# Kernel tuning notes

Hardware: AMD Instinct MI355X
Metric: run time of the kernel (lower is better)

Reference implementation:

```python
import jax, jax.numpy as jnp
import numpy as np

H = 8            # num_heads
HID = 128        # hidden_channels
D = HID // H     # per-head dim
L = 2            # num_layers
NCLS = 4         # out_channels (number of 1-class heads)


def _forward(x_a, x_b, lin_W_a, lin_b_a, lin_W_b, lin_b_b,
             Wk, bk, Wq, bq, Wv, bv, arel, mrel, prel,
             Wa, ba_out, skip, Wcls, bcls, edges):
    """HGT forward. edges: list of (src_type, dst_type, [2,E] int array); list
    position is the relation index into arel/mrel/prel."""
    # per-type input projection + ReLU
    x = [jax.nn.relu(x_a @ lin_W_a + lin_b_a),
         jax.nn.relu(x_b @ lin_W_b + lin_b_b)]
    N = [x[0].shape[0], x[1].shape[0]]
    scale = 1.0 / np.sqrt(D)
    for l in range(L):
        # per-type K/Q/V projections -> [N, H, D]
        k = [(x[t] @ Wk[l, t] + bk[l, t]).reshape(N[t], H, D) for t in range(2)]
        q = [(x[t] @ Wq[l, t] + bq[l, t]).reshape(N[t], H, D) for t in range(2)]
        v = [(x[t] @ Wv[l, t] + bv[l, t]).reshape(N[t], H, D) for t in range(2)]
        new_x = []
        for dt in range(2):
            logits, vals, dsts = [], [], []
            for r, (s_t, d_t, ei) in enumerate(edges):
                if d_t != dt:
                    continue
                src, dst = ei[0], ei[1]
                # relation-specific per-head transforms of gathered src K/V
                ke = jnp.einsum('ehd,hdf->ehf', k[s_t][src], arel[l, r])  # [E,H,D]
                ve = jnp.einsum('ehd,hdf->ehf', v[s_t][src], mrel[l, r])  # [E,H,D]
                a = jnp.sum(q[dt][dst] * ke, axis=-1) * prel[l, r] * scale  # [E,H]
                logits.append(a); vals.append(ve); dsts.append(dst)
            a = jnp.concatenate(logits, axis=0)
            ve = jnp.concatenate(vals, axis=0)
            dst = jnp.concatenate(dsts, axis=0)
            # segment softmax over all incoming edges per destination node
            amax = jax.ops.segment_max(a, dst, num_segments=N[dt])           # [N,H]
            ae = jnp.exp(a - amax[dst])                                       # [E,H]
            den = jax.ops.segment_sum(ae, dst, num_segments=N[dt])           # [N,H]
            msg = jax.ops.segment_sum(ae[:, :, None] * ve, dst,
                                      num_segments=N[dt])                    # [N,H,D]
            out = (msg / jnp.maximum(den, 1e-16)[:, :, None]).reshape(N[dt], HID)
            # output projection with GELU + learned skip gate
            out = jax.nn.gelu(out) @ Wa[l, dt] + ba_out[l, dt]
            beta = jax.nn.sigmoid(skip[l, dt])
            new_x.append(beta * out + (1.0 - beta) * x[dt])
        x = new_x
    # node_to_predict == 'a'; concatenated 1-class heads -> [Na, NCLS]
    return x[0] @ Wcls.T + bcls


def setup_inputs() -> dict:
    key = jax.random.key(0)
    ks = iter(jax.random.split(key, 40))
    Na, Nb, E = 50000, 50000, 150000
    def rn(shape, fan_in):
        return jax.random.normal(next(ks), shape, dtype=jnp.float32) / np.sqrt(fan_in)
    inp = {
        'x_a': jax.random.normal(next(ks), (Na, 64), dtype=jnp.float32),
        'x_b': jax.random.normal(next(ks), (Nb, 32), dtype=jnp.float32),
        'lin_W_a': rn((64, HID), 64), 'lin_b_a': jnp.zeros((HID,), jnp.float32),
        'lin_W_b': rn((32, HID), 32), 'lin_b_b': jnp.zeros((HID,), jnp.float32),
        'Wk': rn((L, 2, HID, HID), HID), 'bk': jnp.zeros((L, 2, HID), jnp.float32),
        'Wq': rn((L, 2, HID, HID), HID), 'bq': jnp.zeros((L, 2, HID), jnp.float32),
        'Wv': rn((L, 2, HID, HID), HID), 'bv': jnp.zeros((L, 2, HID), jnp.float32),
        'arel': rn((L, 4, H, D, D), D), 'mrel': rn((L, 4, H, D, D), D),
        'prel': jnp.ones((L, 4, H), jnp.float32),
        'Wa': rn((L, 2, HID, HID), HID), 'ba_out': jnp.zeros((L, 2, HID), jnp.float32),
        'skip': jnp.ones((L, 2), jnp.float32),
        'Wcls': rn((NCLS, HID), HID), 'bcls': jnp.zeros((NCLS,), jnp.float32),
        'edge_aa': jax.random.randint(next(ks), (2, E), 0, Na, dtype=jnp.int32),
        'edge_ab': jax.random.randint(next(ks), (2, E), 0, Na, dtype=jnp.int32),
        'edge_ba': jax.random.randint(next(ks), (2, E), 0, Na, dtype=jnp.int32),
        'edge_bb': jax.random.randint(next(ks), (2, E), 0, Nb, dtype=jnp.int32),
    }
    return inp


def reference(x_a, x_b, lin_W_a, lin_b_a, lin_W_b, lin_b_b,
              Wk, bk, Wq, bq, Wv, bv, arel, mrel, prel,
              Wa, ba_out, skip, Wcls, bcls,
              edge_aa, edge_ab, edge_ba, edge_bb):
    edges = [(0, 0, edge_aa), (0, 1, edge_ab), (1, 0, edge_ba), (1, 1, edge_bb)]
    return _forward(x_a, x_b, lin_W_a, lin_b_a, lin_W_b, lin_b_b,
                    Wk, bk, Wq, bq, Wv, bv, arel, mrel, prel,
                    Wa, ba_out, skip, Wcls, bcls, edges)
```

## Files before the change

### kernel.cpp

```cpp
#include <hip/hip_runtime.h>
#include <math.h>

#define HIDC 128
#define NH 8
#define HD 16
#define NCLS 4

typedef __attribute__((ext_vector_type(8))) short s8v;
typedef __attribute__((ext_vector_type(4))) float f4v;

#define ST_STRIDE 264
#define ST_BYTES  (64 * ST_STRIDE * 2)

__device__ __forceinline__ float gelu_f(float h) {
    float z = 0.7978845608028654f * (h + 0.044715f * h * h * h);
    float t = 1.f - 2.f / (1.f + __expf(2.f * z));
    return 0.5f * h * (1.f + t);
}
__device__ __forceinline__ unsigned short f2bf(float x) {
    unsigned b = __float_as_uint(x);
    unsigned r = (b + 0x7FFFu + ((b >> 16) & 1u)) >> 16;
    return (unsigned short)r;
}
__device__ __forceinline__ float bf2f(unsigned short u) {
    return __uint_as_float(((unsigned)u) << 16);
}
__device__ __forceinline__ void gload_lds16(const void* g, void* l) {
    __builtin_amdgcn_global_load_lds(
        (const __attribute__((address_space(1))) unsigned int*)g,
        (__attribute__((address_space(3))) unsigned int*)l, 16, 0, 0);
}

__global__ void zero_u32(unsigned* __restrict__ p, long n)
{
    long i = (long)blockIdx.x * blockDim.x + threadIdx.x;
    long stride = (long)gridDim.x * blockDim.x;
    for (; i < n; i += stride) p[i] = 0u;
}

__global__ void fold_all(const float* __restrict__ Wk, const float* __restrict__ bk,
                         const float* __restrict__ Wv, const float* __restrict__ bv,
                         const float* __restrict__ arel, const float* __restrict__ mrel,
                         float* __restrict__ Wt, float* __restrict__ bt)
{
    __shared__ float rsh[NH * HD * HD];
    int bid = blockIdx.x;
    int w = bid & 1, r = (bid >> 1) & 3, l = bid >> 3;
    int st = r >> 1;
    const float* W   = (w ? Wv : Wk) + (size_t)(l * 2 + st) * HIDC * HIDC;
    const float* bb  = (w ? bv : bk) + (size_t)(l * 2 + st) * HIDC;
    const float* rel = (w ? mrel : arel) + (size_t)(l * 4 + r) * NH * HD * HD;
    float* wt  = Wt + (size_t)bid * HIDC * HIDC;
    float* btp = bt + (size_t)bid * HIDC;

    int t = threadIdx.x;
    for (int i = t; i < NH * HD * HD; i += 128) rsh[i] = rel[i];
    __syncthreads();
    int h = t >> 4, f = t & 15;
    const float* rh = rsh + h * HD * HD + f;
    for (int k = 0; k < HIDC; ++k) {
        float acc = 0.f;
        const float* wr = W + (size_t)k * HIDC + h * HD;
        #pragma unroll
        for (int d = 0; d < HD; ++d) acc = fmaf(wr[d], rh[d * HD], acc);
        wt[(size_t)k * HIDC + t] = acc;
    }
    float accb = 0.f;
    const float* br = bb + h * HD;
    #pragma unroll
    for (int d = 0; d < HD; ++d) accb = fmaf(br[d], rh[d * HD], accb);
    btp[t] = accb;
}

__global__ __launch_bounds__(128)
void wsplit(const float* __restrict__ linWa, const float* __restrict__ linWb,
            const float* __restrict__ Wq, const float* __restrict__ Wa,
            const float* __restrict__ Wt, unsigned short* __restrict__ W2,
            int Ka, int Kb)
{
    int bid = blockIdx.x;
    int nka = Ka >> 5, nkb = Kb >> 5;
    const float* src; size_t moff; int ks, Km;
    if (bid < nka) { src = linWa; moff = 0; ks = bid; Km = Ka; }
    else if (bid < nka + nkb) { src = linWb; moff = (size_t)2 * Ka * 128; ks = bid - nka; Km = Kb; }
    else {
        int cc = bid - nka - nkb;
        int mm = cc >> 2; ks = cc & 3; Km = 128;
        moff = (size_t)2 * (Ka + Kb) * 128 + (size_t)mm * 32768;
        if (mm < 16)      src = Wt + (size_t)mm * 16384;
        else if (mm < 20) src = Wq + (size_t)(mm - 16) * 16384;
        else              src = Wa + (size_t)(mm - 20) * 16384;
    }
    int t = threadIdx.x;
    int fn = t >> 4, lr = t & 15;
    for (int g = 0; g < 4; ++g)
        for (int j = 0; j < 8; ++j) {
            int k = ks * 32 + g * 8 + j;
            float x = src[(size_t)k * 128 + fn * 16 + lr];
            unsigned short h = f2bf(x);
            size_t co = moff + (size_t)ks * 4096 + fn * 512 + g * 128 + lr * 8 + j;
            W2[co] = h;
            W2[co + (size_t)Km * 128] = f2bf(x - bf2f(h));
        }
}

__global__ void hist4(const int* __restrict__ d0, int E0, const int* __restrict__ d1, int E1,
                      const int* __restrict__ d2, int E2, const int* __restrict__ d3, int E3,
                      unsigned* __restrict__ cnt, int Nmax)
{
    int i = blockIdx.x * blockDim.x + threadIdx.x;
    int tot = E0 + E1 + E2 + E3;
    int stride = gridDim.x * blockDim.x;
    for (; i < tot; i += stride) {
        int j = i; const int* p; int dt;
        if (j < E0) { p = d0; dt = 0; }
        else { j -= E0;
            if (j < E1) { p = d1; dt = 1; }
            else { j -= E1;
                if (j < E2) { p = d2; dt = 0; }
                else { j -= E2; p = d3; dt = 1; }
            }
        }
        atomicAdd(&cnt[(size_t)dt * Nmax + p[j]], 1u);
    }
}

__global__ __launch_bounds__(256)
void scan_p1(const unsigned* __restrict__ cnt, unsigned* __restrict__ bsum,
             int Nmax, int nblk, int n0, int n1)
{
    int ty = blockIdx.x / nblk, b = blockIdx.x % nblk;
    int n = ty ? n1 : n0;
    const unsigned* c = cnt + (size_t)ty * Nmax;
    int i0 = b * 1024 + threadIdx.x * 4;
    unsigned s = 0;
    #pragma unroll
    for (int j = 0; j < 4; ++j) { int i = i0 + j; if (i < n) s += c[i]; }
    __shared__ unsigned sh[256];
    sh[threadIdx.x] = s; __syncthreads();
    for (int off = 128; off; off >>= 1) {
        if (threadIdx.x < (unsigned)off) sh[threadIdx.x] += sh[threadIdx.x + off];
        __syncthreads();
    }
    if (threadIdx.x == 0) bsum[blockIdx.x] = sh[0];
}

__global__ __launch_bounds__(256)
void scan_p2(unsigned* __restrict__ bsum, int nblk, int* __restrict__ rowptr,
             int Nmax, int n0, int n1)
{
    __shared__ unsigned sh[256];
    int tot = 2 * nblk;
    int t = threadIdx.x;
    unsigned v = (t < tot) ? bsum[t] : 0u;
    sh[t] = v; __syncthreads();
    for (int off = 1; off < 256; off <<= 1) {
        unsigned add = (t >= off) ? sh[t - off] : 0u;
        __syncthreads(); sh[t] += add; __syncthreads();
    }
    unsigned t0 = sh[nblk - 1];
    unsigned tall = sh[255];
    unsigned excl = sh[t] - v;
    if (t < tot) bsum[t] = (t < nblk) ? excl : excl - t0;
    if (t == 0) {
        rowptr[n0] = (int)t0;
        rowptr[(Nmax + 1) + n1] = (int)(tall - t0);
    }
}

__global__ __launch_bounds__(256)
void scan_p3(const unsigned* __restrict__ cnt, const unsigned* __restrict__ bsum,
             int* __restrict__ rowptr, unsigned* __restrict__ cursor,
             int Nmax, int nblk, int n0, int n1)
{
    int ty = blockIdx.x / nblk, b = blockIdx.x % nblk;
    int n = ty ? n1 : n0;
    const unsigned* c = cnt + (size_t)ty * Nmax;
    int* rp = rowptr + (size_t)ty * (Nmax + 1);
    unsigned* cur = cursor + (size_t)ty * Nmax;
    int t = threadIdx.x;
    int i0 = b * 1024 + t * 4;
    unsigned v[4]; unsigned s = 0;
    #pragma unroll
    for (int j = 0; j < 4; ++j) { int i = i0 + j; v[j] = (i < n) ? c[i] : 0u; s += v[j]; }
    __shared__ unsigned sh[256];
    sh[t] = s; __syncthreads();
    for (int off = 1; off < 256; off <<= 1) {
        unsigned add = (t >= off) ? sh[t - off] : 0u;
        __syncthreads(); sh[t] += add; __syncthreads();
    }
    unsigned run = bsum[blockIdx.x] + sh[t] - s;
    #pragma unroll
    for (int j = 0; j < 4; ++j) {
        int i = i0 + j;
        if (i < n) { rp[i] = (int)run; cur[i] = run; }
        run += v[j];
    }
}

__global__ void scatter4(const int* __restrict__ e0, int E0, const int* __restrict__ e1, int E1,
                         const int* __restrict__ e2, int E2, const int* __restrict__ e3, int E3,
                         unsigned* __restrict__ cursor, int Nmax,
                         unsigned* __restrict__ adj0, unsigned* __restrict__ adj1)
{
    int i = blockIdx.x * blockDim.x + threadIdx.x;
    int tot = E0 + E1 + E2 + E3;
    int stride = gridDim.x * blockDim.x;
    for (; i < tot; i += stride) {
        int j = i; const int* e; int E; int dt; unsigned rb;
        if (j < E0) { e = e0; E = E0; dt = 0; rb = 0u; }
        else { j -= E0;
            if (j < E1) { e = e1; E = E1; dt = 1; rb = 0u; }
            else { j -= E1;
                if (j < E2) { e = e2; E = E2; dt = 0; rb = 1u << 24; }
                else { j -= E2; e = e3; E = E3; dt = 1; rb = 1u << 24; }
            }
        }
        int s = e[j], d = e[E + j];
        unsigned pos = atomicAdd(&cursor[(size_t)dt * Nmax + d], 1u);
        (dt ? adj1 : adj0)[pos] = (unsigned)s | rb;
    }
}

template <int ASPLIT, int EPI, int OUT, int NK>
__global__ __launch_bounds__(256)
void mg2p(const void* __restrict__ Ain, const unsigned short* __restrict__ Whi,
          const float* __restrict__ bias,
          const unsigned short* __restrict__ xold, const float* __restrict__ skipp,
          void* __restrict__ Cout, int N)
{
    constexpr int K = NK * 32;
    constexpr int PB = NK * 8192;
    constexpr size_t LSZ = (OUT == 2 && ST_BYTES > PB) ? ST_BYTES : PB;
    __shared__ char ldsraw[LSZ];
    unsigned short* lds = (unsigned short*)ldsraw;
    int t = threadIdx.x;
    constexpr int NCP = PB / (16 * 256);
    #pragma unroll
    for (int i = 0; i < NCP; ++i)
        gload_lds16((const char*)Whi + ((size_t)t + i * 256) * 16,
                    ldsraw + ((size_t)t + i * 256) * 16);
    __syncthreads();

    int w = t >> 6, lane = t & 63;
    int lr = lane & 15, g = lane >> 4;
    int row0 = blockIdx.x * 64;
    int fnb = w * 2;

    f4v acc[4][2];
    #pragma unroll
    for (int i = 0; i < 4; ++i) { acc[i][0] = (f4v)0.f; acc[i][1] = (f4v)0.f; }

    #pragma unroll
    for (int ks = 0; ks < NK; ++ks) {
        s8v ah[4], al[4];
        #pragma unroll
        for (int fm = 0; fm < 4; ++fm) {
            int row = row0 + fm * 16 + lr;
            if (row < N) {
                if (ASPLIT) {
                    const unsigned short* ap = (const unsigned short*)Ain + (size_t)row * 256 + ks * 32 + g * 8;
                    ah[fm] = *(const s8v*)ap;
                    al[fm] = *(const s8v*)(ap + 128);
                } else {
                    const float* ap = (const float*)Ain + (size_t)row * K + ks * 32 + g * 8;
                    float4 p = *(const float4*)ap;
                    float4 q = *(const float4*)(ap + 4);
                    float xv[8] = {p.x, p.y, p.z, p.w, q.x, q.y, q.z, q.w};
                    #pragma unroll
                    for (int j = 0; j < 8; ++j) {
                        unsigned short h = f2bf(xv[j]);
                        ah[fm][j] = (short)h;
                        al[fm][j] = (short)f2bf(xv[j] - bf2f(h));
                    }
                }
            } else { ah[fm] = (s8v)0; al[fm] = (s8v)0; }
        }
        #pragma unroll
        for (int f = 0; f < 2; ++f) {
            size_t co = (size_t)ks * 8192 + (fnb + f) * 1024 + g * 256 + lr * 16;
            s8v b = *(const s8v*)(ldsraw + co);
            #pragma unroll
            for (int fm = 0; fm < 4; ++fm) {
                acc[fm][f] = __builtin_amdgcn_mfma_f32_16x16x32_bf16(ah[fm], b, acc[fm][f], 0, 0, 0);
                acc[fm][f] = __builtin_amdgcn_mfma_f32_16x16x32_bf16(al[fm], b, acc[fm][f], 0, 0, 0);
            }
        }
    }

    float beta = 0.f;
    if (EPI == 2) beta = 1.f / (1.f + __expf(-skipp[0]));
    int rb = g * 4;

    if (OUT == 2) {
        __syncthreads();
        #pragma unroll
        for (int f = 0; f < 2; ++f) {
            int col = (fnb + f) * 16 + lr;
            float bv = bias[col];
            #pragma unroll
            for (int fm = 0; fm < 4; ++fm) {
                #pragma unroll
                for (int j = 0; j < 4; ++j) {
                    int lrow = fm * 16 + rb + j;
                    int row = row0 + lrow;
                    float o = acc[fm][f][j] + bv;
                    if (EPI == 1) o = fmaxf(o, 0.f);
                    if (EPI == 2) {
                        float xo = (row < N) ? (bf2f(xold[(size_t)row * 256 + col]) +
                                                bf2f(xold[(size_t)row * 256 + 128 + col])) : 0.f;
                        o = beta * o + (1.f - beta) * xo;
                    }
                    unsigned short h = f2bf(o);
                    lds[(size_t)lrow * ST_STRIDE + col] = h;
                    lds[(size_t)lrow * ST_STRIDE + 128 + col] = f2bf(o - bf2f(h));
                }
            }
        }
        __syncthreads();
        unsigned short* C = (unsigned short*)Cout;
        #pragma unroll
        for (int it = 0; it < 8; ++it) {
            int d4 = (it * 256 + t) * 4;
            int row = d4 >> 7, c2 = d4 & 127;
            int grow = row0 + row;
            if (grow < N) {
                uint4 v = *(const uint4*)(lds + (size_t)row * ST_STRIDE + c2 * 2);
                *(uint4*)(C + (size_t)grow * 256 + c2 * 2) = v;
            }
        }
    } else {
        float* C = (float*)Cout;
        #pragma unroll
        for (int f = 0; f < 2; ++f) {
            int col = (fnb + f) * 16 + lr;
            float bv = bias[col];
            #pragma unroll
            for (int fm = 0; fm < 4; ++fm) {
                #pragma unroll
                for (int j = 0; j < 4; ++j) {
                    int row = row0 + fm * 16 + rb + j;
                    if (row < N) C[(size_t)row * HIDC + col] = acc[fm][f][j] + bv;
                }
            }
        }
    }
}

struct KvArgs {
    const unsigned short* A[4];
    const unsigned short* Wm[4];
    const float* bias[4];
    unsigned short* out[4];
    int N[4];
    int cum[5];
};

__global__ __launch_bounds__(256)
void mgemm_kv4(KvArgs args)
{
    int bid = blockIdx.x;
    int jb = 0;
    while (jb < 3 && bid >= args.cum[jb + 1]) ++jb;
    int lb = bid - args.cum[jb];
    const unsigned short* Ain = args.A[jb];
    const unsigned short* Wkt = args.Wm[jb];
    const unsigned short* Wvt = args.Wm[jb] + 32768;
    const float* bias2 = args.bias[jb];
    unsigned short* kv = args.out[jb];
    int N = args.N[jb];

    __shared__ char ldsraw[65536];
    unsigned short* lds = (unsigned short*)ldsraw;
    int t = threadIdx.x;
    #pragma unroll
    for (int i = 0; i < 8; ++i)
        gload_lds16((const char*)Wkt + ((size_t)t + i * 256) * 16,
                    ldsraw + ((size_t)t + i * 256) * 16);
    #pragma unroll
    for (int i = 0; i < 8; ++i)
        gload_lds16((const char*)Wvt + ((size_t)t + i * 256) * 16,
                    ldsraw + 32768 + ((size_t)t + i * 256) * 16);

    int w = t >> 6, lane = t & 63;
    int lr = lane & 15, g = lane >> 4;
    int row0 = lb * 64;
    int fnb = w * 2;

    s8v ah[4][4], al[4][4];
    #pragma unroll
    for (int fm = 0; fm < 4; ++fm) {
        int row = row0 + fm * 16 + lr;
        #pragma unroll
        for (int ks = 0; ks < 4; ++ks) {
            if (row < N) {
                const unsigned short* ap = Ain + (size_t)row * 256 + ks * 32 + g * 8;
                ah[fm][ks] = *(const s8v*)ap;
                al[fm][ks] = *(const s8v*)(ap + 128);
            } else { ah[fm][ks] = (s8v)0; al[fm][ks] = (s8v)0; }
        }
    }
    __syncthreads();

    f4v acck[4][2], accv[4][2];
    #pragma unroll
    for (int i = 0; i < 4; ++i) {
        acck[i][0] = (f4v)0.f; acck[i][1] = (f4v)0.f;
        accv[i][0] = (f4v)0.f; accv[i][1] = (f4v)0.f;
    }

    #pragma unroll
    for (int ks = 0; ks < 4; ++ks) {
        #pragma unroll
        for (int f = 0; f < 2; ++f) {
            int fn = fnb + f;
            size_t co = (size_t)ks * 8192 + fn * 1024 + g * 256 + lr * 16;
            s8v bk_ = *(const s8v*)(ldsraw + co);
            s8v bv_ = *(const s8v*)(ldsraw + 32768 + co);
            #pragma unroll
            for (int fm = 0; fm < 4; ++fm) {
                acck[fm][f] = __builtin_amdgcn_mfma_f32_16x16x32_bf16(ah[fm][ks], bk_, acck[fm][f], 0, 0, 0);
                acck[fm][f] = __builtin_amdgcn_mfma_f32_16x16x32_bf16(al[fm][ks], bk_, acck[fm][f], 0, 0, 0);
                accv[fm][f] = __builtin_amdgcn_mfma_f32_16x16x32_bf16(ah[fm][ks], bv_, accv[fm][f], 0, 0, 0);
                accv[fm][f] = __builtin_amdgcn_mfma_f32_16x16x32_bf16(al[fm][ks], bv_, accv[fm][f], 0, 0, 0);
            }
        }
    }

    __syncthreads();
    int rb = g * 4;
    #pragma unroll
    for (int f = 0; f < 2; ++f) {
        int fn = fnb + f;
        int col = fn * 16 + lr;
        float bk0 = bias2[col], bv0 = bias2[128 + col];
        #pragma unroll
        for (int fm = 0; fm < 4; ++fm) {
            #pragma unroll
            for (int j = 0; j < 4; ++j) {
                int lrow = fm * 16 + rb + j;
                lds[(size_t)lrow * ST_STRIDE + col] = f2bf(acck[fm][f][j] + bk0);
                lds[(size_t)lrow * ST_STRIDE + 128 + col] = f2bf(accv[fm][f][j] + bv0);
            }
        }
    }
    __syncthreads();
    #pragma unroll
    for (int it = 0; it < 8; ++it) {
        int d4 = (it * 256 + t) * 4;
        int row = d4 >> 7, c2 = d4 & 127;
        int grow = row0 + row;
        if (grow < N) {
            uint4 v = *(const uint4*)(lds + (size_t)row * ST_STRIDE + c2 * 2);
            *(uint4*)(kv + (size_t)grow * 256 + c2 * 2) = v;
        }
    }
}

struct QArgs {
    const unsigned short* A[2];
    const unsigned short* W[2];
    const float* bias[2];
    float* out[2];
    int N[2];
    int cum[3];
};

__global__ __launch_bounds__(256)
void mgemm_q2(QArgs args)
{
    int bid = blockIdx.x;
    int jb = (bid >= args.cum[1]) ? 1 : 0;
    int lb = bid - args.cum[jb];
    const unsigned short* Ain = args.A[jb];
    const unsigned short* Whi = args.W[jb];
    const float* bias = args.bias[jb];
    float* Cout = args.out[jb];
    int N = args.N[jb];

    __shared__ char ldsraw[32768];
    int t = threadIdx.x;
    #pragma unroll
    for (int i = 0; i < 8; ++i)
        gload_lds16((const char*)Whi + ((size_t)t + i * 256) * 16,
                    ldsraw + ((size_t)t + i * 256) * 16);
    __syncthreads();

    int w = t >> 6, lane = t & 63;
    int lr = lane & 15, g = lane >> 4;
    int row0 = lb * 64;
    int fnb = w * 2;

    f4v acc[4][2];
    #pragma unroll
    for (int i = 0; i < 4; ++i) { acc[i][0] = (f4v)0.f; acc[i][1] = (f4v)0.f; }

    #pragma unroll
    for (int ks = 0; ks < 4; ++ks) {
        s8v ah[4], al[4];
        #pragma unroll
        for (int fm = 0; fm < 4; ++fm) {
            int row = row0 + fm * 16 + lr;
            if (row < N) {
                const unsigned short* ap = Ain + (size_t)row * 256 + ks * 32 + g * 8;
                ah[fm] = *(const s8v*)ap;
                al[fm] = *(const s8v*)(ap + 128);
            } else { ah[fm] = (s8v)0; al[fm] = (s8v)0; }
        }
        #pragma unroll
        for (int f = 0; f < 2; ++f) {
            size_t co = (size_t)ks * 8192 + (fnb + f) * 1024 + g * 256 + lr * 16;
            s8v b = *(const s8v*)(ldsraw + co);
            #pragma unroll
            for (int fm = 0; fm < 4; ++fm) {
                acc[fm][f] = __builtin_amdgcn_mfma_f32_16x16x32_bf16(ah[fm], b, acc[fm][f], 0, 0, 0);
                acc[fm][f] = __builtin_amdgcn_mfma_f32_16x16x32_bf16(al[fm], b, acc[fm][f], 0, 0, 0);
            }
        }
    }

    int rb = g * 4;
    #pragma unroll
    for (int f = 0; f < 2; ++f) {
        int col = (fnb + f) * 16 + lr;
        float bv = bias[col];
        #pragma unroll
        for (int fm = 0; fm < 4; ++fm) {
            #pragma unroll
            for (int j = 0; j < 4; ++j) {
                int row = row0 + fm * 16 + rb + j;
                if (row < N) Cout[(size_t)row * HIDC + col] = acc[fm][f][j] + bv;
            }
        }
    }
}

struct OArgs {
    const unsigned short* A[2];
    const unsigned short* W[2];
    const float* bias[2];
    const float* skipp[2];
    unsigned short* x[2];
    int N[2];
    int cum[3];
};

__global__ __launch_bounds__(256)
void mgemm_op2(OArgs args)
{
    int bid = blockIdx.x;
    int jb = (bid >= args.cum[1]) ? 1 : 0;
    int lb = bid - args.cum[jb];
    const unsigned short* Ain = args.A[jb];
    const unsigned short* Whi = args.W[jb];
    const float* bias = args.bias[jb];
    const unsigned short* xold = args.x[jb];
    unsigned short* Cout = args.x[jb];
    float beta = 1.f / (1.f + __expf(-args.skipp[jb][0]));
    int N = args.N[jb];

    __shared__ char ldsraw[ST_BYTES];
    unsigned short* lds = (unsigned short*)ldsraw;
    int t = threadIdx.x;
    #pragma unroll
    for (int i = 0; i < 8; ++i)
        gload_lds16((const char*)Whi + ((size_t)t + i * 256) * 16,
                    ldsraw + ((size_t)t + i * 256) * 16);
    __syncthreads();

    int w = t >> 6, lane = t & 63;
    int lr = lane & 15, g = lane >> 4;
    int row0 = lb * 64;
    int fnb = w * 2;

    f4v acc[4][2];
    #pragma unroll
    for (int i = 0; i < 4; ++i) { acc[i][0] = (f4v)0.f; acc[i][1] = (f4v)0.f; }

    #pragma unroll
    for (int ks = 0; ks < 4; ++ks) {
        s8v ah[4], al[4];
        #pragma unroll
        for (int fm = 0; fm < 4; ++fm) {
            int row = row0 + fm * 16 + lr;
            if (row < N) {
                const unsigned short* ap = Ain + (size_t)row * 256 + ks * 32 + g * 8;
                ah[fm] = *(const s8v*)ap;
                al[fm] = *(const s8v*)(ap + 128);
            } else { ah[fm] = (s8v)0; al[fm] = (s8v)0; }
        }
        #pragma unroll
        for (int f = 0; f < 2; ++f) {
            size_t co = (size_t)ks * 8192 + (fnb + f) * 1024 + g * 256 + lr * 16;
            s8v b = *(const s8v*)(ldsraw + co);
            #pragma unroll
            for (int fm = 0; fm < 4; ++fm) {
                acc[fm][f] = __builtin_amdgcn_mfma_f32_16x16x32_bf16(ah[fm], b, acc[fm][f], 0, 0, 0);
                acc[fm][f] = __builtin_amdgcn_mfma_f32_16x16x32_bf16(al[fm], b, acc[fm][f], 0, 0, 0);
            }
        }
    }

    int rb = g * 4;
    __syncthreads();
    #pragma unroll
    for (int f = 0; f < 2; ++f) {
        int col = (fnb + f) * 16 + lr;
        float bv = bias[col];
        #pragma unroll
        for (int fm = 0; fm < 4; ++fm) {
            #pragma unroll
            for (int j = 0; j < 4; ++j) {
                int lrow = fm * 16 + rb + j;
                int row = row0 + lrow;
                float o = acc[fm][f][j] + bv;
                float xo = (row < N) ? (bf2f(xold[(size_t)row * 256 + col]) +
                                        bf2f(xold[(size_t)row * 256 + 128 + col])) : 0.f;
                o = beta * o + (1.f - beta) * xo;
                unsigned short h = f2bf(o);
                lds[(size_t)lrow * ST_STRIDE + col] = h;
                lds[(size_t)lrow * ST_STRIDE + 128 + col] = f2bf(o - bf2f(h));
            }
        }
    }
    __syncthreads();
    #pragma unroll
    for (int it = 0; it < 8; ++it) {
        int d4 = (it * 256 + t) * 4;
        int row = d4 >> 7, c2 = d4 & 127;
        int grow = row0 + row;
        if (grow < N) {
            uint4 v = *(const uint4*)(lds + (size_t)row * ST_STRIDE + c2 * 2);
            *(uint4*)(Cout + (size_t)grow * 256 + c2 * 2) = v;
        }
    }
}

#define EDGE_STEP(IDX, M, S, AX, AY)                                               \
    {                                                                              \
        unsigned ent = adj[IDX];                                                   \
        int src = (int)(ent & 0xFFFFFFu);                                          \
        const unsigned short* kv = (ent >> 24) ? kvB : kvA;                        \
        float sp = (ent >> 24) ? spB : spA;                                        \
        ushort2 kraw = *(const ushort2*)(kv + (size_t)src * 256 + lane * 2);       \
        ushort2 vraw = *(const ushort2*)(kv + (size_t)src * 256 + 128 + lane * 2); \
        float p = bf2f(kraw.x) * qv.x + bf2f(kraw.y) * qv.y;                       \
        p += __shfl_xor(p, 1, 8);                                                  \
        p += __shfl_xor(p, 2, 8);                                                  \
        p += __shfl_xor(p, 4, 8);                                                  \
        float a = p * sp;                                                          \
        float mn = fmaxf(M, a);                                                    \
        float cc = __expf(M - mn);                                                 \
        float pe = __expf(a - mn);                                                 \
        S = S * cc + pe;                                                           \
        AX = AX * cc + pe * bf2f(vraw.x);                                          \
        AY = AY * cc + pe * bf2f(vraw.y);                                          \
        M = mn;                                                                    \
    }

struct AArgs {
    const float* Q[2];
    const unsigned short* kvA_[2];
    const unsigned short* kvB_[2];
    const int* rowptr[2];
    const unsigned* adjp[2];
    const float* prelA_[2];
    const float* prelB_[2];
    unsigned short* out[2];
    int N[2];
    int cum[3];
};

__global__ __launch_bounds__(256)
void agg2(AArgs args, float scale)
{
    int bid = blockIdx.x;
    int jb = (bid >= args.cum[1]) ? 1 : 0;
    int lb = bid - args.cum[jb];
    const float* Q = args.Q[jb];
    const unsigned short* kvA = args.kvA_[jb];
    const unsigned short* kvB = args.kvB_[jb];
    const int* rowptr = args.rowptr[jb];
    const unsigned* adj = args.adjp[jb];
    unsigned short* msgs = args.out[jb];
    int N = args.N[jb];

    int node = lb * 4 + (threadIdx.x >> 6);
    if (node >= N) return;
    int lane = threadIdx.x & 63;
    int h = lane >> 3;
    float spA = args.prelA_[jb][h] * scale, spB = args.prelB_[jb][h] * scale;
    float2 qv = *(const float2*)(Q + (size_t)node * HIDC + lane * 2);
    int beg = rowptr[node], end = rowptr[node + 1];

    float m0 = -INFINITY, s0 = 0.f, ax0 = 0.f, ay0 = 0.f;
    float m1 = -INFINITY, s1 = 0.f, ax1 = 0.f, ay1 = 0.f;
    int i = beg;
    for (; i + 1 < end; i += 2) {
        EDGE_STEP(i,     m0, s0, ax0, ay0);
        EDGE_STEP(i + 1, m1, s1, ax1, ay1);
    }
    if (i < end) EDGE_STEP(i, m0, s0, ax0, ay0);

    float ox = 0.f, oy = 0.f;
    if (end > beg) {
        float mn = fmaxf(m0, m1);
        float c0 = __expf(m0 - mn), c1 = __expf(m1 - mn);
        float s = s0 * c0 + s1 * c1;
        float inv = 1.f / fmaxf(s, 1e-16f);
        ox = (ax0 * c0 + ax1 * c1) * inv;
        oy = (ay0 * c0 + ay1 * c1) * inv;
    }
    ox = gelu_f(ox); oy = gelu_f(oy);
    unsigned short hx = f2bf(ox), hy = f2bf(oy);
    size_t base = (size_t)node * 256 + lane * 2;
    ushort2 hi2; hi2.x = hx; hi2.y = hy;
    ushort2 lo2; lo2.x = f2bf(ox - bf2f(hx)); lo2.y = f2bf(oy - bf2f(hy));
    *(ushort2*)(msgs + base) = hi2;
    *(ushort2*)(msgs + base + 128) = lo2;
}

__global__ __launch_bounds__(256)
void cls_kernel(const unsigned short* __restrict__ X, const float* __restrict__ Wc,
                const float* __restrict__ bc, float* __restrict__ out, int N)
{
    int row = blockIdx.x * 4 + (threadIdx.x >> 6);
    if (row >= N) return;
    int lane = threadIdx.x & 63;
    const unsigned short* xr = X + (size_t)row * 256 + lane * 2;
    float x0 = bf2f(xr[0]) + bf2f(xr[128]);
    float x1 = bf2f(xr[1]) + bf2f(xr[129]);
    float p0, p1, p2, p3;
    {
        float2 w0 = *(const float2*)(Wc + 0 * HIDC + lane * 2);
        float2 w1 = *(const float2*)(Wc + 1 * HIDC + lane * 2);
        float2 w2 = *(const float2*)(Wc + 2 * HIDC + lane * 2);
        float2 w3 = *(const float2*)(Wc + 3 * HIDC + lane * 2);
        p0 = x0 * w0.x + x1 * w0.y;
        p1 = x0 * w1.x + x1 * w1.y;
        p2 = x0 * w2.x + x1 * w2.y;
        p3 = x0 * w3.x + x1 * w3.y;
    }
    #pragma unroll
    for (int off = 32; off; off >>= 1) {
        p0 += __shfl_xor(p0, off);
        p1 += __shfl_xor(p1, off);
        p2 += __shfl_xor(p2, off);
        p3 += __shfl_xor(p3, off);
    }
    if (lane < 4) {
        float v = (lane == 0) ? p0 : (lane == 1) ? p1 : (lane == 2) ? p2 : p3;
        out[(size_t)row * NCLS + lane] = v + bc[lane];
    }
}

extern "C" void kernel_launch(void* const* d_in, const int* in_sizes, int n_in,
                              void* d_out, int out_size, void* d_ws, size_t ws_size,
                              hipStream_t stream)
{
    const float* x_a    = (const float*)d_in[0];
    const float* x_b    = (const float*)d_in[1];
    const float* lin_W_a= (const float*)d_in[2];
    const float* lin_b_a= (const float*)d_in[3];
    const float* lin_W_b= (const float*)d_in[4];
    const float* lin_b_b= (const float*)d_in[5];
    const float* Wk     = (const float*)d_in[6];
    const float* bk     = (const float*)d_in[7];
    const float* Wq     = (const float*)d_in[8];
    const float* bq     = (const float*)d_in[9];
    const float* Wv     = (const float*)d_in[10];
    const float* bv     = (const float*)d_in[11];
    const float* arel   = (const float*)d_in[12];
    const float* mrel   = (const float*)d_in[13];
    const float* prel   = (const float*)d_in[14];
    const float* Wa     = (const float*)d_in[15];
    const float* ba     = (const float*)d_in[16];
    const float* skip   = (const float*)d_in[17];
    const float* Wcls   = (const float*)d_in[18];
    const float* bcls   = (const float*)d_in[19];
    const int* eptr[4] = {(const int*)d_in[20], (const int*)d_in[21],
                          (const int*)d_in[22], (const int*)d_in[23]};
    int Ee[4] = {in_sizes[20] / 2, in_sizes[21] / 2, in_sizes[22] / 2, in_sizes[23] / 2};

    int Ka = in_sizes[2] / HIDC;
    int Kb = in_sizes[4] / HIDC;
    int Na = in_sizes[0] / Ka;
    int Nb = in_sizes[1] / Kb;
    int Nn[2] = {Na, Nb};
    int Nmax = Na > Nb ? Na : Nb;

    char* base = (char*)d_ws;
    unsigned short* xs[2];
    xs[0] = (unsigned short*)base; base += (size_t)Na * 256 * 2;
    xs[1] = (unsigned short*)base; base += (size_t)Nb * 256 * 2;
    float* qb[2];
    qb[0] = (float*)base; base += (size_t)Na * HIDC * 4;
    qb[1] = (float*)base; base += (size_t)Nb * HIDC * 4;
    unsigned short* kvb[2][2];
    for (int s = 0; s < 2; ++s)
        for (int d = 0; d < 2; ++d) { kvb[s][d] = (unsigned short*)base; base += (size_t)Nn[s] * 256 * 2; }
    float* Wt = (float*)base; base += (size_t)16 * HIDC * HIDC * 4;
    float* bt = (float*)base; base += (size_t)16 * HIDC * 4;
    size_t nW2 = (size_t)2 * (Ka + Kb) * 128 + (size_t)24 * 32768;
    unsigned short* W2 = (unsigned short*)base; base += nW2 * 2;
    unsigned* cnt = (unsigned*)base; base += (size_t)2 * Nmax * 4;
    unsigned* cursor = (unsigned*)base; base += (size_t)2 * Nmax * 4;
    unsigned* bsum = (unsigned*)base; base += 256 * 4;
    int* rowptr = (int*)base; base += (size_t)2 * (Nmax + 1) * 4;
    unsigned* adj0 = (unsigned*)base; base += (size_t)(Ee[0] + Ee[2]) * 4;
    unsigned* adj1 = (unsigned*)base; base += (size_t)(Ee[1] + Ee[3]) * 4;

    size_t off_lina = 0;
    size_t off_linb = (size_t)2 * Ka * 128;
    size_t base128  = (size_t)2 * (Ka + Kb) * 128;
    auto offKT = [&](int l, int st, int dt) { return base128 + (size_t)(l * 8 + (st * 2 + dt) * 2) * 32768; };
    auto offQ  = [&](int l, int tt) { return base128 + (size_t)(16 + l * 2 + tt) * 32768; };
    auto offA  = [&](int l, int tt) { return base128 + (size_t)(20 + l * 2 + tt) * 32768; };

    fold_all<<<16, 128, 0, stream>>>(Wk, bk, Wv, bv, arel, mrel, Wt, bt);
    int nwblk = (Ka >> 5) + (Kb >> 5) + 24 * 4;
    wsplit<<<nwblk, 128, 0, stream>>>(lin_W_a, lin_W_b, Wq, Wa, Wt, W2, Ka, Kb);

    int nblk = (Nmax + 1023) / 1024;
    zero_u32<<<512, 256, 0, stream>>>(cnt, (long)2 * Nmax);
    hist4<<<1024, 256, 0, stream>>>(eptr[0] + Ee[0], Ee[0], eptr[1] + Ee[1], Ee[1],
                                    eptr[2] + Ee[2], Ee[2], eptr[3] + Ee[3], Ee[3],
                                    cnt, Nmax);
    scan_p1<<<2 * nblk, 256, 0, stream>>>(cnt, bsum, Nmax, nblk, Na, Nb);
    scan_p2<<<1, 256, 0, stream>>>(bsum, nblk, rowptr, Nmax, Na, Nb);
    scan_p3<<<2 * nblk, 256, 0, stream>>>(cnt, bsum, rowptr, cursor, Nmax, nblk, Na, Nb);
    scatter4<<<1024, 256, 0, stream>>>(eptr[0], Ee[0], eptr[1], Ee[1],
                                       eptr[2], Ee[2], eptr[3], Ee[3],
                                       cursor, Nmax, adj0, adj1);

    int gn64[2] = {(Na + 63) / 64, (Nb + 63) / 64};
    mg2p<0, 1, 2, 2><<<gn64[0], 256, 0, stream>>>(x_a, W2 + off_lina, lin_b_a,
                                                  nullptr, nullptr, xs[0], Na);
    mg2p<0, 1, 2, 1><<<gn64[1], 256, 0, stream>>>(x_b, W2 + off_linb, lin_b_b,
                                                  nullptr, nullptr, xs[1], Nb);

    const float scale = 0.25f;
    int ganode[2] = {(Na + 3) / 4, (Nb + 3) / 4};

    for (int l = 0; l < 2; ++l) {
        KvArgs ka;
        int cum = 0;
        for (int j = 0; j < 4; ++j) {
            int st = j >> 1, dt = j & 1;
            int bid = l * 8 + (st * 2 + dt) * 2;
            ka.A[j] = xs[st];
            ka.Wm[j] = W2 + offKT(l, st, dt);
            ka.bias[j] = bt + (size_t)bid * HIDC;
            ka.out[j] = kvb[st][dt];
            ka.N[j] = Nn[st];
            ka.cum[j] = cum;
            cum += gn64[st];
        }
        ka.cum[4] = cum;
        mgemm_kv4<<<cum, 256, 0, stream>>>(ka);

        QArgs qa;
        for (int j = 0; j < 2; ++j) {
            qa.A[j] = xs[j];
            qa.W[j] = W2 + offQ(l, j);
            qa.bias[j] = bq + (l * 2 + j) * HIDC;
            qa.out[j] = qb[j];
            qa.N[j] = Nn[j];
        }
        qa.cum[0] = 0; qa.cum[1] = gn64[0]; qa.cum[2] = gn64[0] + gn64[1];
        mgemm_q2<<<qa.cum[2], 256, 0, stream>>>(qa);

        AArgs aa;
        aa.Q[0] = qb[0]; aa.Q[1] = qb[1];
        aa.kvA_[0] = kvb[0][0]; aa.kvB_[0] = kvb[1][0];
        aa.kvA_[1] = kvb[0][1]; aa.kvB_[1] = kvb[1][1];
        aa.rowptr[0] = rowptr; aa.rowptr[1] = rowptr + (Nmax + 1);
        aa.adjp[0] = adj0; aa.adjp[1] = adj1;
        aa.prelA_[0] = prel + (l * 4 + 0) * NH; aa.prelB_[0] = prel + (l * 4 + 2) * NH;
        aa.prelA_[1] = prel + (l * 4 + 1) * NH; aa.prelB_[1] = prel + (l * 4 + 3) * NH;
        aa.out[0] = (unsigned short*)qb[0]; aa.out[1] = (unsigned short*)qb[1];
        aa.N[0] = Nn[0]; aa.N[1] = Nn[1];
        aa.cum[0] = 0; aa.cum[1] = ganode[0]; aa.cum[2] = ganode[0] + ganode[1];
        agg2<<<aa.cum[2], 256, 0, stream>>>(aa, scale);

        OArgs oa;
        for (int j = 0; j < 2; ++j) {
            oa.A[j] = (const unsigned short*)qb[j];
            oa.W[j] = W2 + offA(l, j);
            oa.bias[j] = ba + (l * 2 + j) * HIDC;
            oa.skipp[j] = skip + (l * 2 + j);
            oa.x[j] = xs[j];
            oa.N[j] = Nn[j];
        }
        oa.cum[0] = 0; oa.cum[1] = gn64[0]; oa.cum[2] = gn64[0] + gn64[1];
        mgemm_op2<<<oa.cum[2], 256, 0, stream>>>(oa);
    }

    cls_kernel<<<(Na + 3) / 4, 256, 0, stream>>>(xs[0], Wcls, bcls, (float*)d_out, Na);
}
```

Measured before the change: 592.2 us.

## Process two edges per wavefront in aggregation with 4-wide lanes and single-exp online softmax

```diff
diff --git a/kernel.cpp b/kernel.cpp
--- a/kernel.cpp
+++ b/kernel.cpp
@@ -11,6 +11,7 @@
 
 #define ST_STRIDE 264
 #define ST_BYTES  (64 * ST_STRIDE * 2)
+#define MNEG (-3.0e38f)
 
 __device__ __forceinline__ float gelu_f(float h) {
     float z = 0.7978845608028654f * (h + 0.044715f * h * h * h);
@@ -636,28 +637,6 @@
     }
 }
 
-#define EDGE_STEP(IDX, M, S, AX, AY)                                               \
-    {                                                                              \
-        unsigned ent = adj[IDX];                                                   \
-        int src = (int)(ent & 0xFFFFFFu);                                          \
-        const unsigned short* kv = (ent >> 24) ? kvB : kvA;                        \
-        float sp = (ent >> 24) ? spB : spA;                                        \
-        ushort2 kraw = *(const ushort2*)(kv + (size_t)src * 256 + lane * 2);       \
-        ushort2 vraw = *(const ushort2*)(kv + (size_t)src * 256 + 128 + lane * 2); \
-        float p = bf2f(kraw.x) * qv.x + bf2f(kraw.y) * qv.y;                       \
-        p += __shfl_xor(p, 1, 8);                                                  \
-        p += __shfl_xor(p, 2, 8);                                                  \
-        p += __shfl_xor(p, 4, 8);                                                  \
-        float a = p * sp;                                                          \
-        float mn = fmaxf(M, a);                                                    \
-        float cc = __expf(M - mn);                                                 \
-        float pe = __expf(a - mn);                                                 \
-        S = S * cc + pe;                                                           \
-        AX = AX * cc + pe * bf2f(vraw.x);                                          \
-        AY = AY * cc + pe * bf2f(vraw.y);                                          \
-        M = mn;                                                                    \
-    }
-
 struct AArgs {
     const float* Q[2];
     const unsigned short* kvA_[2];
@@ -688,36 +667,90 @@
     int node = lb * 4 + (threadIdx.x >> 6);
     if (node >= N) return;
     int lane = threadIdx.x & 63;
-    int h = lane >> 3;
+    int e2 = lane >> 5;
+    int sub = lane & 31;
+    int h = sub >> 2;
+    int off = h * 16 + (sub & 3) * 4;
     float spA = args.prelA_[jb][h] * scale, spB = args.prelB_[jb][h] * scale;
-    float2 qv = *(const float2*)(Q + (size_t)node * HIDC + lane * 2);
+
+    float4 qv = *(const float4*)(Q + (size_t)node * HIDC + off);
     int beg = rowptr[node], end = rowptr[node + 1];
 
-    float m0 = -INFINITY, s0 = 0.f, ax0 = 0.f, ay0 = 0.f;
-    float m1 = -INFINITY, s1 = 0.f, ax1 = 0.f, ay1 = 0.f;
+    float m0 = MNEG, s0 = 0.f, v00 = 0.f, v01 = 0.f, v02 = 0.f, v03 = 0.f;
+    float m1 = MNEG, s1 = 0.f, v10 = 0.f, v11 = 0.f, v12 = 0.f, v13 = 0.f;
+
+#define ESTEP(I, M, S, A0, A1, A2, A3)                                            \
+    {                                                                             \
+        int ei = (I) + e2;                                                        \
+        bool valid = ei < end;                                                    \
+        unsigned ent = valid ? adj[ei] : 0u;                                      \
+        int src = (int)(ent & 0xFFFFFFu);                                         \
+        const unsigned short* kvp = (ent >> 24) ? kvB : kvA;                      \
+        float sp = (ent >> 24) ? spB : spA;                                       \
+        ushort4 kr = *(const ushort4*)(kvp + (size_t)src * 256 + off);            \
+        ushort4 vr = *(const ushort4*)(kvp + (size_t)src * 256 + 128 + off);      \
+        float p = bf2f(kr.x) * qv.x + bf2f(kr.y) * qv.y +                         \
+                  bf2f(kr.z) * qv.z + bf2f(kr.w) * qv.w;                          \
+        p += __shfl_xor(p, 1, 4);                                                 \
+        p += __shfl_xor(p, 2, 4);                                                 \
+        float a = p * sp;                                                         \
+        float d = a - M;                                                          \
+        float e = __expf(-fabsf(d));                                              \
+        bool nm = valid && (d > 0.f);                                             \
+        float sc = nm ? e : 1.f;                                                  \
+        float pw = nm ? 1.f : e;                                                  \
+        pw = valid ? pw : 0.f;                                                    \
+        S = S * sc + pw;                                                          \
+        A0 = A0 * sc + pw * bf2f(vr.x);                                           \
+        A1 = A1 * sc + pw * bf2f(vr.y);                                           \
+        A2 = A2 * sc + pw * bf2f(vr.z);                                           \
+        A3 = A3 * sc + pw * bf2f(vr.w);                                           \
+        M = nm ? a : M;                                                           \
+    }
+
     int i = beg;
-    for (; i + 1 < end; i += 2) {
-        EDGE_STEP(i,     m0, s0, ax0, ay0);
-        EDGE_STEP(i + 1, m1, s1, ax1, ay1);
-    }
-    if (i < end) EDGE_STEP(i, m0, s0, ax0, ay0);
-
-    float ox = 0.f, oy = 0.f;
+    for (; i + 3 < end; i += 4) {
+        ESTEP(i,     m0, s0, v00, v01, v02, v03);
+        ESTEP(i + 2, m1, s1, v10, v11, v12, v13);
+    }
+    if (i < end) { ESTEP(i, m0, s0, v00, v01, v02, v03); i += 2; }
+    if (i < end) { ESTEP(i, m1, s1, v10, v11, v12, v13); }
+
+    float o0 = 0.f, o1 = 0.f, o2 = 0.f, o3 = 0.f;
     if (end > beg) {
-        float mn = fmaxf(m0, m1);
-        float c0 = __expf(m0 - mn), c1 = __expf(m1 - mn);
-        float s = s0 * c0 + s1 * c1;
+        float mm = fmaxf(m0, m1);
+        float c0 = __expf(m0 - mm), c1 = __expf(m1 - mm);
+        float ss = s0 * c0 + s1 * c1;
+        float b0 = v00 * c0 + v10 * c1;
+        float b1 = v01 * c0 + v11 * c1;
+        float b2 = v02 * c0 + v12 * c1;
+        float b3 = v03 * c0 + v13 * c1;
+        float om = __shfl_xor(mm, 32);
+        float os = __shfl_xor(ss, 32);
+        float ob0 = __shfl_xor(b0, 32);
+        float ob1 = __shfl_xor(b1, 32);
+        float ob2 = __shfl_xor(b2, 32);
+        float ob3 = __shfl_xor(b3, 32);
+        float mn = fmaxf(mm, om);
+        float d0 = __expf(mm - mn), d1 = __expf(om - mn);
+        float s = ss * d0 + os * d1;
         float inv = 1.f / fmaxf(s, 1e-16f);
-        ox = (ax0 * c0 + ax1 * c1) * inv;
-        oy = (ay0 * c0 + ay1 * c1) * inv;
-    }
-    ox = gelu_f(ox); oy = gelu_f(oy);
-    unsigned short hx = f2bf(ox), hy = f2bf(oy);
-    size_t base = (size_t)node * 256 + lane * 2;
-    ushort2 hi2; hi2.x = hx; hi2.y = hy;
-    ushort2 lo2; lo2.x = f2bf(ox - bf2f(hx)); lo2.y = f2bf(oy - bf2f(hy));
-    *(ushort2*)(msgs + base) = hi2;
-    *(ushort2*)(msgs + base + 128) = lo2;
+        o0 = (b0 * d0 + ob0 * d1) * inv;
+        o1 = (b1 * d0 + ob1 * d1) * inv;
+        o2 = (b2 * d0 + ob2 * d1) * inv;
+        o3 = (b3 * d0 + ob3 * d1) * inv;
+    }
+    o0 = gelu_f(o0); o1 = gelu_f(o1); o2 = gelu_f(o2); o3 = gelu_f(o3);
+    if (e2 == 0) {
+        ushort4 hi, lo;
+        hi.x = f2bf(o0); lo.x = f2bf(o0 - bf2f(hi.x));
+        hi.y = f2bf(o1); lo.y = f2bf(o1 - bf2f(hi.y));
+        hi.z = f2bf(o2); lo.z = f2bf(o2 - bf2f(hi.z));
+        hi.w = f2bf(o3); lo.w = f2bf(o3 - bf2f(hi.w));
+        *(ushort4*)(msgs + (size_t)node * 256 + off) = hi;
+        *(ushort4*)(msgs + (size_t)node * 256 + 128 + off) = lo;
+    }
+#undef ESTEP
 }
 
 __global__ __launch_bounds__(256)
```

Result: no change. 599.1 us (+1.2%).
